# Optimization experiments

Measured on AMD Instinct MI355X. Metric: run time of the kernel, lower is better.

Reference implementation:

```python
import jax, jax.numpy as jnp
import numpy as np

N = 100000      # nodes
E = 3200000     # edges per graph (pos and neg)
IN_FEATS = 128
HIDDEN = 32
PROP_STEP = 8
USE_RELU = False  # args.relu default False


def setup_inputs() -> dict:
    key = jax.random.key(0)
    ks = jax.random.split(key, 8)
    in_feat = jax.random.normal(ks[0], (N, IN_FEATS), dtype=jnp.float32)
    src = jax.random.randint(ks[1], (E,), 0, N, dtype=jnp.int32)
    dst = jax.random.randint(ks[2], (E,), 0, N, dtype=jnp.int32)
    neg_src = jax.random.randint(ks[3], (E,), 0, N, dtype=jnp.int32)
    neg_dst = jax.random.randint(ks[4], (E,), 0, N, dtype=jnp.int32)
    W1 = jax.random.normal(ks[5], (IN_FEATS, HIDDEN), dtype=jnp.float32) * (1.0 / np.sqrt(IN_FEATS))
    b1 = jnp.zeros((HIDDEN,), dtype=jnp.float32)
    gamma = jnp.ones((HIDDEN,), dtype=jnp.float32)
    beta = jnp.zeros((HIDDEN,), dtype=jnp.float32)
    W2 = jax.random.normal(ks[6], (HIDDEN, HIDDEN), dtype=jnp.float32) * (1.0 / np.sqrt(HIDDEN))
    b2 = jnp.zeros((HIDDEN,), dtype=jnp.float32)
    return dict(in_feat=in_feat, W1=W1, b1=b1, gamma=gamma, beta=beta,
                W2=W2, b2=b2, src=src, dst=dst, neg_src=neg_src, neg_dst=neg_dst)


def _graph_conv(h, src, dst, n_nodes):
    """DGL GraphConv(norm='both', weight=False, bias=False):
       out = D_dst^{-1/2} A D_src^{-1/2} h, sum aggregation."""
    ones = jnp.ones(src.shape, dtype=h.dtype)
    out_deg = jax.ops.segment_sum(ones, src, num_segments=n_nodes)
    in_deg = jax.ops.segment_sum(ones, dst, num_segments=n_nodes)
    hs = h * jax.lax.rsqrt(jnp.clip(out_deg, 1.0))[:, None]   # [N, H]
    msg = hs[src]                                             # [E, H] gather
    agg = jax.ops.segment_sum(msg, dst, num_segments=n_nodes)  # [N, H] scatter-add
    return agg * jax.lax.rsqrt(jnp.clip(in_deg, 1.0))[:, None]


def reference(in_feat, W1, b1, gamma, beta, W2, b2, src, dst, neg_src, neg_dst):
    # MLP: Linear -> BatchNorm1d (training-mode batch stats) -> (Dropout noop) -> ReLU -> Linear
    x = in_feat @ W1 + b1
    mu = jnp.mean(x, axis=0)
    var = jnp.var(x, axis=0)
    x = (x - mu) * jax.lax.rsqrt(var + 1e-5) * gamma + beta
    x = jax.nn.relu(x)
    ori_h = x @ W2 + b2                                       # [N, H]

    # Iterative pos-neg SpMM propagation with residual (h initialized to ori_h)
    h = ori_h
    for _ in range(PROP_STEP):
        if USE_RELU:
            h = jax.nn.relu(h)
        h = _graph_conv(h, src, dst, N) - _graph_conv(h, neg_src, neg_dst, N) + ori_h
    return h
```

## Files before the change

kernel.cpp:

```cpp
#include <hip/hip_runtime.h>
#include <hip/hip_fp16.h>

#define N_NODES 100000
#define E_EDGES 3200000
#define IN_F 128
#define HID 32
#define PROP 8

#define WIN 32768
#define NWIN 4
#define HS 32

#define MB_ROWS 64
#define MB_BLOCKS ((N_NODES + MB_ROWS - 1) / MB_ROWS)
#define RED_B 32

#define FB 1024
#define CH 6250
#define BK_SH 7
#define BK_N 128
#define NBK 782
#define L2S (NBK * FB)
#define SCB2 782
#define STG 12288

__global__ __launch_bounds__(256) void hist_kernel(const int* __restrict__ s,
        const int* __restrict__ ns, int* __restrict__ degs) {
    __shared__ int lh[WIN];
    int b = blockIdx.x;
    int w = b % NWIN;
    int st = (b / NWIN) % 2;
    int sl = b / (NWIN * 2);
    const int* p = st ? ns : s;
    for (int i = threadIdx.x; i < WIN; i += 256) lh[i] = 0;
    __syncthreads();
    const int lo = w * WIN;
    const int per = E_EDGES / HS;
    const int4* p4 = (const int4*)(p + sl * per);
    for (int i = threadIdx.x; i < per / 4; i += 256) {
        int4 v = p4[i];
        int a;
        a = v.x - lo; if ((unsigned)a < WIN) atomicAdd(&lh[a], 1);
        a = v.y - lo; if ((unsigned)a < WIN) atomicAdd(&lh[a], 1);
        a = v.z - lo; if ((unsigned)a < WIN) atomicAdd(&lh[a], 1);
        a = v.w - lo; if ((unsigned)a < WIN) atomicAdd(&lh[a], 1);
    }
    __syncthreads();
    int* g = degs + st * N_NODES;
    for (int i = threadIdx.x; i < WIN; i += 256) {
        int idx = lo + i;
        if (idx < N_NODES && lh[i]) atomicAdd(&g[idx], lh[i]);
    }
}

__global__ void inv_sqrt_kernel(const int* __restrict__ deg, float* __restrict__ inv, int n) {
    int i = blockIdx.x * blockDim.x + threadIdx.x;
    if (i < n) inv[i] = rsqrtf(fmaxf((float)deg[i], 1.0f));
}

__global__ __launch_bounds__(256) void countA_kernel(const int* __restrict__ dst,
        const int* __restrict__ ndst, int* __restrict__ counts) {
    __shared__ int lh[NBK];
    int blk = blockIdx.x;
    for (int i = threadIdx.x; i < NBK; i += 256) lh[i] = 0;
    __syncthreads();
    const int* dp = (blk < FB / 2) ? dst + blk * CH : ndst + (blk - FB / 2) * CH;
    const int2* dp2 = (const int2*)dp;
    for (int i = threadIdx.x; i < CH / 2; i += 256) {
        int2 v = dp2[i];
        atomicAdd(&lh[v.x >> BK_SH], 1);
        atomicAdd(&lh[v.y >> BK_SH], 1);
    }
    __syncthreads();
    for (int b = threadIdx.x; b < NBK; b += 256) counts[b * FB + blk] = lh[b];
}

__global__ __launch_bounds__(1024) void scanA2_kernel(const int* __restrict__ counts,
        int* __restrict__ offs, int* __restrict__ blockSums) {
    __shared__ int sh[1024];
    int t = threadIdx.x, b = blockIdx.x;
    int i = b * 1024 + t;
    int v = counts[i];
    sh[t] = v;
    __syncthreads();
    for (int off = 1; off < 1024; off <<= 1) {
        int u = (t >= off) ? sh[t - off] : 0;
        __syncthreads();
        sh[t] += u;
        __syncthreads();
    }
    offs[i] = sh[t] - v;
    if (t == 1023) blockSums[b] = sh[1023];
}

__global__ __launch_bounds__(1024) void scanB2_kernel(const int* __restrict__ blockSums,
        int* __restrict__ blockOff) {
    __shared__ int sh[1024];
    int t = threadIdx.x;
    int v = (t < SCB2) ? blockSums[t] : 0;
    sh[t] = v;
    __syncthreads();
    for (int off = 1; off < 1024; off <<= 1) {
        int u = (t >= off) ? sh[t - off] : 0;
        __syncthreads();
        sh[t] += u;
        __syncthreads();
    }
    if (t < SCB2) blockOff[t] = sh[t] - v;
}

__global__ __launch_bounds__(1024) void scanC2_kernel(int* __restrict__ offs,
        const int* __restrict__ blockOff) {
    int b = blockIdx.x, t = threadIdx.x;
    int i = b * 1024 + t;
    offs[i] += blockOff[b];
    if (i == 0) offs[L2S] = 2 * E_EDGES;
}

__global__ __launch_bounds__(256) void fillA2_kernel(const int* __restrict__ src, const int* __restrict__ dst,
        const int* __restrict__ nsrc, const int* __restrict__ ndst,
        const float* __restrict__ invs, const int* __restrict__ offs, int2* __restrict__ rec) {
    __shared__ int cur[NBK];
    __shared__ int base[NBK];
    int blk = blockIdx.x;
    int g = (blk >= FB / 2);
    const int* sp = g ? (nsrc + (blk - FB / 2) * CH) : (src + blk * CH);
    const int* dp = g ? (ndst + (blk - FB / 2) * CH) : (dst + blk * CH);
    const float* io = invs + (g ? N_NODES : 0);
    const float sign = g ? -1.f : 1.f;
    const int gbit = g << 24;
    for (int i = threadIdx.x; i < NBK; i += 256) {
        cur[i] = 0;
        base[i] = offs[i * FB + blk];
    }
    __syncthreads();
    for (int i = threadIdx.x; i < CH; i += 256) {
        int u = sp[i], v = dp[i];
        int b = v >> BK_SH;
        float c = sign * io[u];
        int p = base[b] + atomicAdd(&cur[b], 1);
        rec[p] = make_int2(u | ((v & (BK_N - 1)) << 17) | gbit, __float_as_int(c));
    }
}

__global__ __launch_bounds__(256) void reorder_kernel(const int* __restrict__ offs,
        const int2* __restrict__ rec, int2* __restrict__ rec2, int* __restrict__ row_ptr2) {
    __shared__ int cnt[BK_N];
    __shared__ int cntp[BK_N];
    __shared__ int scn[BK_N];
    __shared__ int lbase[BK_N];
    __shared__ float invp[BK_N], invn[BK_N];
    __shared__ int2 stage[STG];
    int bkt = blockIdx.x, tid = threadIdx.x;
    if (tid < BK_N) { cnt[tid] = 0; cntp[tid] = 0; }
    __syncthreads();
    int beg = offs[bkt * FB], end = offs[(bkt + 1) * FB];
    for (int i = beg + tid; i < end; i += 256) {
        int rx = rec[i].x;
        int d = (rx >> 17) & (BK_N - 1);
        atomicAdd(&cnt[d], 1);
        if (!(rx & (1 << 24))) atomicAdd(&cntp[d], 1);
    }
    __syncthreads();
    int v = (tid < BK_N) ? cnt[tid] : 0;
    if (tid < BK_N) {
        scn[tid] = v;
        int np = cntp[tid];
        invp[tid] = rsqrtf(fmaxf((float)np, 1.0f));
        invn[tid] = rsqrtf(fmaxf((float)(v - np), 1.0f));
    }
    __syncthreads();
    for (int off = 1; off < BK_N; off <<= 1) {
        int u = (tid < BK_N && tid >= off) ? scn[tid - off] : 0;
        __syncthreads();
        if (tid < BK_N) scn[tid] += u;
        __syncthreads();
    }
    if (tid < BK_N) {
        int b = scn[tid] - v;
        lbase[tid] = b;
        row_ptr2[bkt * BK_N + tid] = beg + b;
        cnt[tid] = 0;
    }
    if (bkt == NBK - 1 && tid == 0) row_ptr2[NBK * BK_N] = 2 * E_EDGES;
    __syncthreads();
    for (int i = beg + tid; i < end; i += 256) {
        int2 r = rec[i];
        int d = (r.x >> 17) & (BK_N - 1);
        int g = (r.x >> 24) & 1;
        float c = __int_as_float(r.y) * (g ? invn[d] : invp[d]);
        int p = lbase[d] + atomicAdd(&cnt[d], 1);
        stage[p] = make_int2(r.x & 0x1FFFF, __float_as_int(c));
    }
    __syncthreads();
    int n = end - beg;
    for (int j = tid; j < n; j += 256) rec2[beg + j] = stage[j];
}

__global__ __launch_bounds__(256) void mlp1_kernel(const float* __restrict__ in_feat,
        const float* __restrict__ W1, const float* __restrict__ b1,
        float* __restrict__ x, float* __restrict__ partials) {
    __shared__ float4 sRow4[MB_ROWS * 32];
    __shared__ float  sW1t[32 * 132];
    int tid = threadIdx.x;
    for (int idx = tid; idx < IN_F * HID; idx += 256) {
        int j = idx >> 5, k = idx & 31;
        sW1t[k * 132 + j] = W1[idx];
    }
    int nb = blockIdx.x * MB_ROWS;
    const float4* inf4 = (const float4*)in_feat;
    for (int idx = tid; idx < MB_ROWS * 32; idx += 256) {
        int row = idx >> 5, q = idx & 31;
        int g = nb + row;
        float4 v = (g < N_NODES) ? inf4[(size_t)g * 32 + q] : make_float4(0.f, 0.f, 0.f, 0.f);
        sRow4[row * 32 + (q ^ (row & 31))] = v;
    }
    __syncthreads();
    int rt = tid & 31, kt = tid >> 5;
    int k0 = kt * 4;
    float acc[2][4] = {{0.f}};
    const float4* w0p = (const float4*)&sW1t[(k0 + 0) * 132];
    const float4* w1p = (const float4*)&sW1t[(k0 + 1) * 132];
    const float4* w2p = (const float4*)&sW1t[(k0 + 2) * 132];
    const float4* w3p = (const float4*)&sW1t[(k0 + 3) * 132];
    #pragma unroll 4
    for (int jq = 0; jq < 32; ++jq) {
        int pq = jq ^ rt;
        float4 a0 = sRow4[rt * 32 + pq];
        float4 a1 = sRow4[(rt + 32) * 32 + pq];
        float4 w0 = w0p[jq], w1 = w1p[jq], w2 = w2p[jq], w3 = w3p[jq];
        acc[0][0] += a0.x*w0.x + a0.y*w0.y + a0.z*w0.z + a0.w*w0.w;
        acc[0][1] += a0.x*w1.x + a0.y*w1.y + a0.z*w1.z + a0.w*w1.w;
        acc[0][2] += a0.x*w2.x + a0.y*w2.y + a0.z*w2.z + a0.w*w2.w;
        acc[0][3] += a0.x*w3.x + a0.y*w3.y + a0.z*w3.z + a0.w*w3.w;
        acc[1][0] += a1.x*w0.x + a1.y*w0.y + a1.z*w0.z + a1.w*w0.w;
        acc[1][1] += a1.x*w1.x + a1.y*w1.y + a1.z*w1.z + a1.w*w1.w;
        acc[1][2] += a1.x*w2.x + a1.y*w2.y + a1.z*w2.z + a1.w*w2.w;
        acc[1][3] += a1.x*w3.x + a1.y*w3.y + a1.z*w3.z + a1.w*w3.w;
    }
    float bb[4] = { b1[k0], b1[k0 + 1], b1[k0 + 2], b1[k0 + 3] };
    float s[4] = {0.f, 0.f, 0.f, 0.f}, ss[4] = {0.f, 0.f, 0.f, 0.f};
    #pragma unroll
    for (int i = 0; i < 2; ++i) {
        int row = nb + rt + 32 * i;
        if (row < N_NODES) {
            float4 o;
            o.x = acc[i][0] + bb[0];
            o.y = acc[i][1] + bb[1];
            o.z = acc[i][2] + bb[2];
            o.w = acc[i][3] + bb[3];
            *(float4*)&x[(size_t)row * HID + k0] = o;
            s[0] += o.x; ss[0] += o.x * o.x;
            s[1] += o.y; ss[1] += o.y * o.y;
            s[2] += o.z; ss[2] += o.z * o.z;
            s[3] += o.w; ss[3] += o.w * o.w;
        }
    }
    for (int off = 16; off; off >>= 1) {
        #pragma unroll
        for (int c = 0; c < 4; ++c) {
            s[c]  += __shfl_down(s[c],  off, 32);
            ss[c] += __shfl_down(ss[c], off, 32);
        }
    }
    if (rt == 0) {
        float* pb = partials + (size_t)blockIdx.x * 64;
        #pragma unroll
        for (int c = 0; c < 4; ++c) {
            pb[k0 + c]      = s[c];
            pb[32 + k0 + c] = ss[c];
        }
    }
}

__global__ __launch_bounds__(256) void bnred_kernel(const float* __restrict__ partials,
        float* __restrict__ partials2) {
    __shared__ float red[4][64];
    int t = threadIdx.x, b = blockIdx.x;
    int r = t >> 6, c = t & 63;
    float sum = 0.f;
    for (int g = b * 4 + r; g < MB_BLOCKS; g += RED_B * 4)
        sum += partials[(size_t)g * 64 + c];
    red[r][c] = sum;
    __syncthreads();
    if (t < 64) partials2[b * 64 + t] = (red[0][t] + red[1][t]) + (red[2][t] + red[3][t]);
}

__global__ __launch_bounds__(256) void bnparam_kernel(const float* __restrict__ partials2,
        const float* __restrict__ gamma, const float* __restrict__ beta, float* __restrict__ params) {
    __shared__ float red[4][64];
    int t = threadIdx.x;
    int col = t & 63, ch = t >> 6;
    float sum = 0.f;
    for (int g = ch; g < RED_B; g += 4) sum += partials2[(size_t)g * 64 + col];
    red[ch][col] = sum;
    __syncthreads();
    if (t < 64) red[0][t] = red[0][t] + red[1][t] + red[2][t] + red[3][t];
    __syncthreads();
    if (t < HID) {
        float mu  = red[0][t] * (1.0f / (float)N_NODES);
        float var = red[0][t + 32] * (1.0f / (float)N_NODES) - mu * mu;
        float sg = gamma[t] * rsqrtf(var + 1e-5f);
        params[t]       = sg;
        params[HID + t] = beta[t] - mu * sg;
    }
}

__global__ __launch_bounds__(256) void mlp2_kernel(const float* __restrict__ x,
        const float* __restrict__ params, const float* __restrict__ W2,
        const float* __restrict__ b2, float* __restrict__ ori_h, __half* __restrict__ h16) {
    __shared__ float sW2[HID * HID];
    __shared__ float sXn[8][HID];
    int tid = threadIdx.x;
    for (int i = tid; i < HID * HID; i += 256) sW2[i] = W2[i];
    int nb = blockIdx.x * 8;
    int k = tid & 31, r = tid >> 5;
    float v = x[(size_t)(nb + r) * HID + k];
    v = fmaxf(fmaf(v, params[k], params[HID + k]), 0.f);
    sXn[r][k] = v;
    __syncthreads();
    float acc = b2[k];
    #pragma unroll
    for (int j = 0; j < HID; ++j) acc = fmaf(sXn[r][j], sW2[j * HID + k], acc);
    int o = (nb + r) * HID + k;
    ori_h[o] = acc;
    h16[o] = __float2half(acc);
}

__device__ __forceinline__ float2 h2f(int b) {
    __half2 h; __builtin_memcpy(&h, &b, 4); return __half22float2(h);
}

__global__ __launch_bounds__(256) void gather_kernel(const int* __restrict__ row_ptr,
        const int2* __restrict__ rec, const int4* __restrict__ h4,
        const float4* __restrict__ ori4, int4* __restrict__ hn4, float4* __restrict__ out4) {
    int tid = threadIdx.x;
    int node = blockIdx.x * 8 + (tid >> 5);
    int lane = tid & 31;
    int slot = lane >> 2;
    int ql = lane & 3;
    int beg = row_ptr[node], end = row_ptr[node + 1];
    float2 a0 = {0.f, 0.f}, a1 = {0.f, 0.f}, a2 = {0.f, 0.f}, a3 = {0.f, 0.f};
    int i = beg;
#define ACC8(f, c) { float2 u_; \
        u_ = h2f((f).x); a0.x = fmaf((c), u_.x, a0.x); a0.y = fmaf((c), u_.y, a0.y); \
        u_ = h2f((f).y); a1.x = fmaf((c), u_.x, a1.x); a1.y = fmaf((c), u_.y, a1.y); \
        u_ = h2f((f).z); a2.x = fmaf((c), u_.x, a2.x); a2.y = fmaf((c), u_.y, a2.y); \
        u_ = h2f((f).w); a3.x = fmaf((c), u_.x, a3.x); a3.y = fmaf((c), u_.y, a3.y); }
    for (; i + 32 <= end; i += 32) {
        int2 r0 = rec[i + slot];
        int2 r1 = rec[i + 8 + slot];
        int2 r2 = rec[i + 16 + slot];
        int2 r3 = rec[i + 24 + slot];
        int4 f0 = h4[r0.x * 4 + ql];
        int4 f1 = h4[r1.x * 4 + ql];
        int4 f2 = h4[r2.x * 4 + ql];
        int4 f3 = h4[r3.x * 4 + ql];
        float c0 = __int_as_float(r0.y), c1 = __int_as_float(r1.y);
        float c2 = __int_as_float(r2.y), c3 = __int_as_float(r3.y);
        ACC8(f0, c0) ACC8(f1, c1) ACC8(f2, c2) ACC8(f3, c3)
    }
    for (; i + 8 <= end; i += 8) {
        int2 r = rec[i + slot];
        int4 f = h4[r.x * 4 + ql];
        float c = __int_as_float(r.y);
        ACC8(f, c)
    }
    if (i + slot < end) {
        int2 r = rec[i + slot];
        int4 f = h4[r.x * 4 + ql];
        float c = __int_as_float(r.y);
        ACC8(f, c)
    }
#undef ACC8
    #pragma unroll
    for (int off = 4; off <= 16; off <<= 1) {
        a0.x += __shfl_down(a0.x, off, 32); a0.y += __shfl_down(a0.y, off, 32);
        a1.x += __shfl_down(a1.x, off, 32); a1.y += __shfl_down(a1.y, off, 32);
        a2.x += __shfl_down(a2.x, off, 32); a2.y += __shfl_down(a2.y, off, 32);
        a3.x += __shfl_down(a3.x, off, 32); a3.y += __shfl_down(a3.y, off, 32);
    }
    if (slot == 0) {
        float4 oA = ori4[node * 8 + ql * 2];
        float4 oB = ori4[node * 8 + ql * 2 + 1];
        float r0x = a0.x + oA.x, r0y = a0.y + oA.y;
        float r1x = a1.x + oA.z, r1y = a1.y + oA.w;
        float r2x = a2.x + oB.x, r2y = a2.y + oB.y;
        float r3x = a3.x + oB.z, r3y = a3.y + oB.w;
        if (out4) {
            out4[node * 8 + ql * 2]     = make_float4(r0x, r0y, r1x, r1y);
            out4[node * 8 + ql * 2 + 1] = make_float4(r2x, r2y, r3x, r3y);
        } else {
            __half2 p0 = __floats2half2_rn(r0x, r0y);
            __half2 p1 = __floats2half2_rn(r1x, r1y);
            __half2 p2 = __floats2half2_rn(r2x, r2y);
            __half2 p3 = __floats2half2_rn(r3x, r3y);
            int4 w;
            __builtin_memcpy(&w.x, &p0, 4);
            __builtin_memcpy(&w.y, &p1, 4);
            __builtin_memcpy(&w.z, &p2, 4);
            __builtin_memcpy(&w.w, &p3, 4);
            hn4[node * 4 + ql] = w;
        }
    }
}

extern "C" void kernel_launch(void* const* d_in, const int* in_sizes, int n_in,
                              void* d_out, int out_size, void* d_ws, size_t ws_size,
                              hipStream_t stream) {
    const float* in_feat = (const float*)d_in[0];
    const float* W1    = (const float*)d_in[1];
    const float* b1    = (const float*)d_in[2];
    const float* gamma = (const float*)d_in[3];
    const float* beta  = (const float*)d_in[4];
    const float* W2    = (const float*)d_in[5];
    const float* b2    = (const float*)d_in[6];
    const int* src  = (const int*)d_in[7];
    const int* dst  = (const int*)d_in[8];
    const int* nsrc = (const int*)d_in[9];
    const int* ndst = (const int*)d_in[10];
    float* out = (float*)d_out;

    float* ws      = (float*)d_ws;
    float* x       = ws;
    float* ori_h   = x + (size_t)N_NODES * HID;
    float* invs    = ori_h + (size_t)N_NODES * HID;
    float* params  = invs + 2 * (size_t)N_NODES;
    float* partials= params + 2 * HID;
    float* partials2 = partials + (size_t)MB_BLOCKS * 64;
    int*   degs    = (int*)(partials2 + (size_t)RED_B * 64);
    int*   offs    = degs + 2 * N_NODES;
    int*   blockSums = offs + L2S + 2;
    int*   blockOff  = blockSums + 1024;
    int*   row_ptr2  = blockOff + 1024;
    uintptr_t hp  = (uintptr_t)(row_ptr2 + NBK * BK_N + 2);
    hp = (hp + 63) & ~(uintptr_t)63;
    __half* h16A   = (__half*)hp;
    __half* h16B   = h16A + (size_t)N_NODES * HID;
    uintptr_t rp  = (uintptr_t)(h16B + (size_t)N_NODES * HID);
    rp = (rp + 63) & ~(uintptr_t)63;
    int2*  rec    = (int2*)rp;
    int*   counts = (int*)x;
    int2*  rec2   = (int2*)in_feat;

    hipMemsetAsync(degs, 0, 2 * (size_t)N_NODES * sizeof(int), stream);

    hist_kernel<<<NWIN * 2 * HS, 256, 0, stream>>>(src, nsrc, degs);
    inv_sqrt_kernel<<<(2 * N_NODES + 255) / 256, 256, 0, stream>>>(degs, invs, 2 * N_NODES);

    countA_kernel<<<FB, 256, 0, stream>>>(dst, ndst, counts);
    scanA2_kernel<<<SCB2, 1024, 0, stream>>>(counts, offs, blockSums);
    scanB2_kernel<<<1, 1024, 0, stream>>>(blockSums, blockOff);
    scanC2_kernel<<<SCB2, 1024, 0, stream>>>(offs, blockOff);
    fillA2_kernel<<<FB, 256, 0, stream>>>(src, dst, nsrc, ndst, invs, offs, rec);

    mlp1_kernel<<<MB_BLOCKS, 256, 0, stream>>>(in_feat, W1, b1, x, partials);
    bnred_kernel<<<RED_B, 256, 0, stream>>>(partials, partials2);
    bnparam_kernel<<<1, 256, 0, stream>>>(partials2, gamma, beta, params);
    mlp2_kernel<<<N_NODES / 8, 256, 0, stream>>>(x, params, W2, b2, ori_h, h16A);

    reorder_kernel<<<NBK, 256, 0, stream>>>(offs, rec, rec2, row_ptr2);

    const __half* h = h16A;
    for (int it = 0; it < PROP; ++it) {
        __half* hn16 = (it & 1) ? h16A : h16B;
        float* o32 = (it == PROP - 1) ? out : nullptr;
        gather_kernel<<<N_NODES / 8, 256, 0, stream>>>(row_ptr2, rec2,
                (const int4*)h, (const float4*)ori_h, (int4*)hn16, (float4*)o32);
        h = hn16;
    }
}
```

Baseline: 980.0 us.

## Shrink bucket records to 4 bytes and defer source-norm lookup to reorder

The first-level bucket fill now writes a 4-byte packed index instead of an 8-byte index-plus-coefficient pair. The source-degree normalisation and the negative sign are now applied in the reorder kernel, where the node index is decoded. Fill blocks are halved with twice the chunk size, which shrinks the count matrix and the scans, and the count kernel reads int4 instead of int2. This cuts the global write and read traffic of the intermediate records and the scan work, but moves a random invs gather into reorder and gives fewer, larger fill blocks.

After: 980.0 us. About the same (-0.0%).

```diff
diff --git a/kernel.cpp b/kernel.cpp
--- a/kernel.cpp
+++ b/kernel.cpp
@@ -15,13 +15,13 @@
 #define MB_BLOCKS ((N_NODES + MB_ROWS - 1) / MB_ROWS)
 #define RED_B 32
 
-#define FB 1024
-#define CH 6250
+#define FB 512
+#define CH 12500
 #define BK_SH 7
 #define BK_N 128
 #define NBK 782
 #define L2S (NBK * FB)
-#define SCB2 782
+#define SCB2 391
 #define STG 12288
 
 __global__ __launch_bounds__(256) void hist_kernel(const int* __restrict__ s,
@@ -65,11 +65,13 @@
     for (int i = threadIdx.x; i < NBK; i += 256) lh[i] = 0;
     __syncthreads();
     const int* dp = (blk < FB / 2) ? dst + blk * CH : ndst + (blk - FB / 2) * CH;
-    const int2* dp2 = (const int2*)dp;
-    for (int i = threadIdx.x; i < CH / 2; i += 256) {
-        int2 v = dp2[i];
+    const int4* dp4 = (const int4*)dp;
+    for (int i = threadIdx.x; i < CH / 4; i += 256) {
+        int4 v = dp4[i];
         atomicAdd(&lh[v.x >> BK_SH], 1);
         atomicAdd(&lh[v.y >> BK_SH], 1);
+        atomicAdd(&lh[v.z >> BK_SH], 1);
+        atomicAdd(&lh[v.w >> BK_SH], 1);
     }
     __syncthreads();
     for (int b = threadIdx.x; b < NBK; b += 256) counts[b * FB + blk] = lh[b];
@@ -93,14 +95,14 @@
     if (t == 1023) blockSums[b] = sh[1023];
 }
 
-__global__ __launch_bounds__(1024) void scanB2_kernel(const int* __restrict__ blockSums,
+__global__ __launch_bounds__(512) void scanB2_kernel(const int* __restrict__ blockSums,
         int* __restrict__ blockOff) {
-    __shared__ int sh[1024];
+    __shared__ int sh[512];
     int t = threadIdx.x;
     int v = (t < SCB2) ? blockSums[t] : 0;
     sh[t] = v;
     __syncthreads();
-    for (int off = 1; off < 1024; off <<= 1) {
+    for (int off = 1; off < 512; off <<= 1) {
         int u = (t >= off) ? sh[t - off] : 0;
         __syncthreads();
         sh[t] += u;
@@ -119,15 +121,13 @@
 
 __global__ __launch_bounds__(256) void fillA2_kernel(const int* __restrict__ src, const int* __restrict__ dst,
         const int* __restrict__ nsrc, const int* __restrict__ ndst,
-        const float* __restrict__ invs, const int* __restrict__ offs, int2* __restrict__ rec) {
+        const int* __restrict__ offs, int* __restrict__ rec) {
     __shared__ int cur[NBK];
     __shared__ int base[NBK];
     int blk = blockIdx.x;
     int g = (blk >= FB / 2);
     const int* sp = g ? (nsrc + (blk - FB / 2) * CH) : (src + blk * CH);
     const int* dp = g ? (ndst + (blk - FB / 2) * CH) : (dst + blk * CH);
-    const float* io = invs + (g ? N_NODES : 0);
-    const float sign = g ? -1.f : 1.f;
     const int gbit = g << 24;
     for (int i = threadIdx.x; i < NBK; i += 256) {
         cur[i] = 0;
@@ -137,14 +137,14 @@
     for (int i = threadIdx.x; i < CH; i += 256) {
         int u = sp[i], v = dp[i];
         int b = v >> BK_SH;
-        float c = sign * io[u];
         int p = base[b] + atomicAdd(&cur[b], 1);
-        rec[p] = make_int2(u | ((v & (BK_N - 1)) << 17) | gbit, __float_as_int(c));
+        rec[p] = u | ((v & (BK_N - 1)) << 17) | gbit;
     }
 }
 
 __global__ __launch_bounds__(256) void reorder_kernel(const int* __restrict__ offs,
-        const int2* __restrict__ rec, int2* __restrict__ rec2, int* __restrict__ row_ptr2) {
+        const int* __restrict__ rec, const float* __restrict__ invs,
+        int2* __restrict__ rec2, int* __restrict__ row_ptr2) {
     __shared__ int cnt[BK_N];
     __shared__ int cntp[BK_N];
     __shared__ int scn[BK_N];
@@ -156,7 +156,7 @@
     __syncthreads();
     int beg = offs[bkt * FB], end = offs[(bkt + 1) * FB];
     for (int i = beg + tid; i < end; i += 256) {
-        int rx = rec[i].x;
+        int rx = rec[i];
         int d = (rx >> 17) & (BK_N - 1);
         atomicAdd(&cnt[d], 1);
         if (!(rx & (1 << 24))) atomicAdd(&cntp[d], 1);
@@ -185,12 +185,14 @@
     if (bkt == NBK - 1 && tid == 0) row_ptr2[NBK * BK_N] = 2 * E_EDGES;
     __syncthreads();
     for (int i = beg + tid; i < end; i += 256) {
-        int2 r = rec[i];
-        int d = (r.x >> 17) & (BK_N - 1);
-        int g = (r.x >> 24) & 1;
-        float c = __int_as_float(r.y) * (g ? invn[d] : invp[d]);
+        int rx = rec[i];
+        int d = (rx >> 17) & (BK_N - 1);
+        int g = (rx >> 24) & 1;
+        int u = rx & 0x1FFFF;
+        float io = invs[u + (g ? N_NODES : 0)];
+        float c = (g ? -io : io) * (g ? invn[d] : invp[d]);
         int p = lbase[d] + atomicAdd(&cnt[d], 1);
-        stage[p] = make_int2(r.x & 0x1FFFF, __float_as_int(c));
+        stage[p] = make_int2(u, __float_as_int(c));
     }
     __syncthreads();
     int n = end - beg;
@@ -431,15 +433,15 @@
     int*   degs    = (int*)(partials2 + (size_t)RED_B * 64);
     int*   offs    = degs + 2 * N_NODES;
     int*   blockSums = offs + L2S + 2;
-    int*   blockOff  = blockSums + 1024;
-    int*   row_ptr2  = blockOff + 1024;
+    int*   blockOff  = blockSums + 512;
+    int*   row_ptr2  = blockOff + 512;
     uintptr_t hp  = (uintptr_t)(row_ptr2 + NBK * BK_N + 2);
     hp = (hp + 63) & ~(uintptr_t)63;
     __half* h16A   = (__half*)hp;
     __half* h16B   = h16A + (size_t)N_NODES * HID;
     uintptr_t rp  = (uintptr_t)(h16B + (size_t)N_NODES * HID);
     rp = (rp + 63) & ~(uintptr_t)63;
-    int2*  rec    = (int2*)rp;
+    int*   rec    = (int*)rp;
     int*   counts = (int*)x;
     int2*  rec2   = (int2*)in_feat;
 
@@ -450,16 +452,16 @@
 
     countA_kernel<<<FB, 256, 0, stream>>>(dst, ndst, counts);
     scanA2_kernel<<<SCB2, 1024, 0, stream>>>(counts, offs, blockSums);
-    scanB2_kernel<<<1, 1024, 0, stream>>>(blockSums, blockOff);
+    scanB2_kernel<<<1, 512, 0, stream>>>(blockSums, blockOff);
     scanC2_kernel<<<SCB2, 1024, 0, stream>>>(offs, blockOff);
-    fillA2_kernel<<<FB, 256, 0, stream>>>(src, dst, nsrc, ndst, invs, offs, rec);
+    fillA2_kernel<<<FB, 256, 0, stream>>>(src, dst, nsrc, ndst, offs, rec);
 
     mlp1_kernel<<<MB_BLOCKS, 256, 0, stream>>>(in_feat, W1, b1, x, partials);
     bnred_kernel<<<RED_B, 256, 0, stream>>>(partials, partials2);
     bnparam_kernel<<<1, 256, 0, stream>>>(partials2, gamma, beta, params);
     mlp2_kernel<<<N_NODES / 8, 256, 0, stream>>>(x, params, W2, b2, ori_h, h16A);
 
-    reorder_kernel<<<NBK, 256, 0, stream>>>(offs, rec, rec2, row_ptr2);
+    reorder_kernel<<<NBK, 256, 0, stream>>>(offs, rec, invs, rec2, row_ptr2);
 
     const __half* h = h16A;
     for (int it = 0; it < PROP; ++it) {
```
